# Kernel tuning notes

Measured on AMD Instinct MI355X. Metric: run time of the kernel, lower is better.

## Reference

```python
import jax, jax.numpy as jnp
import numpy as np

B, L, F = 512, 30, 64
N_LEADERS, MAX_LAG = 500, 10
H, TOP_K = 64, 5
SCALE = float(H) ** 0.5


def setup_inputs() -> dict:
    key = jax.random.key(0)
    ks = jax.random.split(key, 16)
    s = 0.05
    return {
        "target_seq": jax.random.normal(ks[0], (B, L, F), jnp.float32),
        "leader_raw_features": jax.random.normal(ks[1], (B, N_LEADERS, MAX_LAG, F), jnp.float32),
        # LSTM params (torch gate order i,f,g,o)
        "W_ih": jax.random.normal(ks[2], (4 * H, F), jnp.float32) * s,
        "W_hh": jax.random.normal(ks[3], (4 * H, H), jnp.float32) * s,
        "b_ih": jax.random.normal(ks[4], (4 * H,), jnp.float32) * s,
        "b_hh": jax.random.normal(ks[5], (4 * H,), jnp.float32) * s,
        # attention projections (bias-free)
        "W_Q": jax.random.normal(ks[6], (H, H), jnp.float32) * s,
        "W_K": jax.random.normal(ks[7], (H, F), jnp.float32) * s,
        # predictor MLP: F->H, H->H//2, H//2->1
        "Wp1": jax.random.normal(ks[8], (H, F), jnp.float32) * s,
        "bp1": jax.random.normal(ks[9], (H,), jnp.float32) * s,
        "Wp2": jax.random.normal(ks[10], (H // 2, H), jnp.float32) * s,
        "bp2": jax.random.normal(ks[11], (H // 2,), jnp.float32) * s,
        "Wp3": jax.random.normal(ks[12], (1, H // 2), jnp.float32) * s,
        "bp3": jax.random.normal(ks[13], (1,), jnp.float32) * s,
    }


def _lstm_last_hidden(x, W_ih, W_hh, b_ih, b_hh):
    # x: [B, L, F] -> last hidden state [B, H]
    b = x.shape[0]
    h0 = jnp.zeros((b, W_hh.shape[1]), x.dtype)

    def step(carry, xt):
        h, c = carry
        gates = xt @ W_ih.T + h @ W_hh.T + b_ih + b_hh  # [B, 4H]
        i, f, g, o = jnp.split(gates, 4, axis=-1)
        i = jax.nn.sigmoid(i)
        f = jax.nn.sigmoid(f)
        g = jnp.tanh(g)
        o = jax.nn.sigmoid(o)
        c = f * c + i * g
        h = o * jnp.tanh(c)
        return (h, c), None

    (h_last, _), _ = jax.lax.scan(step, (h0, h0), jnp.swapaxes(x, 0, 1))
    return h_last


def reference(target_seq, leader_raw_features, W_ih, W_hh, b_ih, b_hh,
              W_Q, W_K, Wp1, bp1, Wp2, bp2, Wp3, bp3):
    b = target_seq.shape[0]
    n_leaders, max_lag, feat = leader_raw_features.shape[1:]

    h_last = _lstm_last_hidden(target_seq, W_ih, W_hh, b_ih, b_hh)  # [B,H]
    query = h_last @ W_Q.T  # [B,H]

    # attn[b,n,l] = sum_h query[b,h] * (W_K @ raw[b,n,l])_h, fused to avoid
    # materializing the [B,N,LAG,H] key tensor.
    attn = jnp.einsum('bnlf,hf,bh->bnl', leader_raw_features, W_K, query) / SCALE

    flat_attn = attn.reshape(b, n_leaders * max_lag)
    k = min(TOP_K, flat_attn.shape[1])
    top_values, top_idx = jax.lax.top_k(flat_attn, k)  # [B,k]
    leader_idx = top_idx // max_lag
    lag_idx = top_idx % max_lag
    top_k_indices = jnp.stack([leader_idx, lag_idx], axis=-1)  # [B,k,2]
    top_k_scores = jax.nn.softmax(top_values, axis=-1)  # [B,k]

    raw_flat = leader_raw_features.reshape(b, n_leaders * max_lag, feat)
    selected = jnp.take_along_axis(raw_flat, top_idx[:, :, None], axis=1)  # [B,k,F]
    weighted = jnp.einsum('bkf,bk->bf', selected, top_k_scores)  # [B,F]

    # predictor MLP (dropout is identity in eval)
    h1 = jax.nn.relu(weighted @ Wp1.T + bp1)
    h2 = jax.nn.relu(h1 @ Wp2.T + bp2)
    pred = h2 @ Wp3.T + bp3  # [B,1]
    return pred, top_k_indices, top_k_scores, attn
```

## Files before the change

kernel.cpp:

```cpp
#include <hip/hip_runtime.h>
#include <math.h>

#define B_SZ   512
#define L_SEQ  30
#define F_DIM  64
#define N_LEAD 500
#define MAXLAG 10
#define H_DIM  64
#define NROWS  5000
#define TOPK   5

#define OFF_IDX   512
#define OFF_SCORE 5632
#define OFF_ATTN  8192

typedef float v4f __attribute__((ext_vector_type(4)));

__device__ __forceinline__ float fast_sigmoid(float x) {
    return 1.f / (1.f + __expf(-x));
}
__device__ __forceinline__ float fast_tanh(float x) {
    float ax = fabsf(x);
    float t  = __expf(-2.f * ax);
    float r  = (1.f - t) / (1.f + t);
    return copysignf(r, x);
}

__device__ __forceinline__ float dot16(const float4* __restrict__ w,
                                       const float4* __restrict__ v) {
    float a0 = 0.f, a1 = 0.f, a2 = 0.f, a3 = 0.f;
#pragma unroll
    for (int k = 0; k < 16; k += 4) {
        a0 += w[k+0].x*v[k+0].x + w[k+0].y*v[k+0].y + w[k+0].z*v[k+0].z + w[k+0].w*v[k+0].w;
        a1 += w[k+1].x*v[k+1].x + w[k+1].y*v[k+1].y + w[k+1].z*v[k+1].z + w[k+1].w*v[k+1].w;
        a2 += w[k+2].x*v[k+2].x + w[k+2].y*v[k+2].y + w[k+2].z*v[k+2].z + w[k+2].w*v[k+2].w;
        a3 += w[k+3].x*v[k+3].x + w[k+3].y*v[k+3].y + w[k+3].z*v[k+3].z + w[k+3].w*v[k+3].w;
    }
    return (a0 + a1) + (a2 + a3);
}

__global__ __launch_bounds__(256) void lstm_kq_kernel(
    const float* __restrict__ x,
    const float* __restrict__ W_ih,
    const float* __restrict__ W_hh,
    const float* __restrict__ b_ih,
    const float* __restrict__ b_hh,
    const float* __restrict__ W_Q,
    const float* __restrict__ W_K,
    float* __restrict__ kq)
{
    __shared__ __align__(16) float xs[L_SEQ * F_DIM];
    __shared__ __align__(16) float hs[H_DIM];
    __shared__ __align__(16) float gates[256];

    const int b = blockIdx.x;
    const int t = threadIdx.x;

    for (int i = t; i < L_SEQ * F_DIM; i += 256)
        xs[i] = x[b * L_SEQ * F_DIM + i];
    if (t < H_DIM) hs[t] = 0.f;

    float4 wih[16], whh[16];
    const float4* wihp = (const float4*)(W_ih + t * 64);
    const float4* whhp = (const float4*)(W_hh + t * 64);
#pragma unroll
    for (int k = 0; k < 16; ++k) { wih[k] = wihp[k]; whh[k] = whhp[k]; }
    const float bsum = b_ih[t] + b_hh[t];

    float c = 0.f;
    __syncthreads();

    float gx = bsum + dot16(wih, (const float4*)xs);

    for (int step = 0; step < L_SEQ; ++step) {
        float g = gx + dot16(whh, (const float4*)hs);
        gates[t] = g;
        __syncthreads();
        if (t < H_DIM) {
            float ig = fast_sigmoid(gates[t]);
            float fg = fast_sigmoid(gates[t + 64]);
            float gg = fast_tanh(gates[t + 128]);
            float og = fast_sigmoid(gates[t + 192]);
            c = fg * c + ig * gg;
            hs[t] = og * fast_tanh(c);
        }
        if (step + 1 < L_SEQ)
            gx = bsum + dot16(wih, (const float4*)(xs + (step + 1) * F_DIM));
        __syncthreads();
    }

    if (t < H_DIM)
        gates[t] = dot16((const float4*)(W_Q + t * 64), (const float4*)hs);
    __syncthreads();
    if (t < F_DIM) {
        float a0 = 0.f, a1 = 0.f;
        for (int h = 0; h < H_DIM; h += 2) {
            a0 += gates[h]     * W_K[h * F_DIM + t];
            a1 += gates[h + 1] * W_K[(h + 1) * F_DIM + t];
        }
        kq[b * F_DIM + t] = a0 + a1;
    }
}

#define CHUNKS 10
#define ROWS_PER_BLK 500
__global__ __launch_bounds__(256) void attn_kernel(
    const float* __restrict__ raw,
    const float* __restrict__ kq,
    float* __restrict__ attn)
{
    const int b     = blockIdx.x / CHUNKS;
    const int chunk = blockIdx.x % CHUNKS;
    const int sub   = threadIdx.x & 15;
    const int rg    = threadIdx.x >> 4;

    const float4 kqv = ((const float4*)(kq + b * 64))[sub];
    const int base   = chunk * ROWS_PER_BLK;
    const size_t rowb = (size_t)b * NROWS;

    for (int it = 0; it < 8; ++it) {
#pragma unroll
        for (int j = 0; j < 4; ++j) {
            int row = base + it * 64 + j * 16 + rg;
            if (row < base + ROWS_PER_BLK) {
                const v4f* pp = (const v4f*)(raw + ((rowb + row) << 6)) + sub;
                v4f v = __builtin_nontemporal_load(pp);
                float s = v.x * kqv.x + v.y * kqv.y + v.z * kqv.z + v.w * kqv.w;
                s += __shfl_xor(s, 8);
                s += __shfl_xor(s, 4);
                s += __shfl_xor(s, 2);
                s += __shfl_xor(s, 1);
                if (sub == 0) attn[rowb + row] = s * 0.125f;
            }
        }
    }
}

__global__ __launch_bounds__(256) void topk_mlp_kernel(
    const float* __restrict__ attn,
    const float* __restrict__ raw,
    const float* __restrict__ Wp1, const float* __restrict__ bp1,
    const float* __restrict__ Wp2, const float* __restrict__ bp2,
    const float* __restrict__ Wp3, const float* __restrict__ bp3,
    float* __restrict__ out)
{
    __shared__ __align__(16) float av[NROWS];
    __shared__ float redv[4];
    __shared__ int   redi[4];
    __shared__ float topv[TOPK];
    __shared__ int   topi[TOPK];
    __shared__ float sc[TOPK];
    __shared__ __align__(16) float wsum[64];
    __shared__ __align__(16) float h1[64];
    __shared__ float h2[32];

    const int b = blockIdx.x, t = threadIdx.x;

    const float4* ain = (const float4*)(attn + (size_t)b * NROWS);
    float4* av4 = (float4*)av;
    for (int i = t; i < NROWS / 4; i += 256) av4[i] = ain[i];
    __syncthreads();

    for (int pp = 0; pp < TOPK; ++pp) {
        float bv = -INFINITY; int bi = 0x7fffffff;
        for (int i = t; i < NROWS; i += 256) {
            float v = av[i];
            if (v > bv || (v == bv && i < bi)) { bv = v; bi = i; }
        }
#pragma unroll
        for (int m = 32; m >= 1; m >>= 1) {
            float ov = __shfl_xor(bv, m);
            int   oi = __shfl_xor(bi, m);
            if (ov > bv || (ov == bv && oi < bi)) { bv = ov; bi = oi; }
        }
        if ((t & 63) == 0) { redv[t >> 6] = bv; redi[t >> 6] = bi; }
        __syncthreads();
        if (t == 0) {
            for (int w = 1; w < 4; ++w)
                if (redv[w] > bv || (redv[w] == bv && redi[w] < bi)) { bv = redv[w]; bi = redi[w]; }
            topv[pp] = bv; topi[pp] = bi;
            av[bi] = -INFINITY;
        }
        __syncthreads();
    }

    if (t == 0) {
        float mx = topv[0];
        float e[TOPK], s = 0.f;
#pragma unroll
        for (int k = 0; k < TOPK; ++k) { e[k] = __expf(topv[k] - mx); s += e[k]; }
        float inv = 1.f / s;
#pragma unroll
        for (int k = 0; k < TOPK; ++k) {
            sc[k] = e[k] * inv;
            out[OFF_IDX + b * 10 + 2 * k]     = (float)(topi[k] / MAXLAG);
            out[OFF_IDX + b * 10 + 2 * k + 1] = (float)(topi[k] % MAXLAG);
            out[OFF_SCORE + b * TOPK + k]     = sc[k];
        }
    }
    __syncthreads();

    if (t < 64) {
        float acc = 0.f;
#pragma unroll
        for (int k = 0; k < TOPK; ++k)
            acc += sc[k] * raw[((size_t)b * NROWS + topi[k]) * 64 + t];
        wsum[t] = acc;
    }
    __syncthreads();
    if (t < 64) {
        float a = bp1[t];
        const float4* w = (const float4*)(Wp1 + t * 64);
        const float4* v = (const float4*)wsum;
#pragma unroll
        for (int k = 0; k < 16; ++k)
            a += w[k].x*v[k].x + w[k].y*v[k].y + w[k].z*v[k].z + w[k].w*v[k].w;
        h1[t] = fmaxf(a, 0.f);
    }
    __syncthreads();
    if (t < 32) {
        float a = bp2[t];
        const float4* w = (const float4*)(Wp2 + t * 64);
        const float4* v = (const float4*)h1;
#pragma unroll
        for (int k = 0; k < 16; ++k)
            a += w[k].x*v[k].x + w[k].y*v[k].y + w[k].z*v[k].z + w[k].w*v[k].w;
        h2[t] = fmaxf(a, 0.f);
    }
    __syncthreads();
    if (t == 0) {
        float a = bp3[0];
#pragma unroll
        for (int f = 0; f < 32; ++f) a += Wp3[f] * h2[f];
        out[b] = a;
    }
}

extern "C" void kernel_launch(void* const* d_in, const int* in_sizes, int n_in,
                              void* d_out, int out_size, void* d_ws, size_t ws_size,
                              hipStream_t stream) {
    const float* target = (const float*)d_in[0];
    const float* raw    = (const float*)d_in[1];
    const float* W_ih   = (const float*)d_in[2];
    const float* W_hh   = (const float*)d_in[3];
    const float* b_ih   = (const float*)d_in[4];
    const float* b_hh   = (const float*)d_in[5];
    const float* W_Q    = (const float*)d_in[6];
    const float* W_K    = (const float*)d_in[7];
    const float* Wp1    = (const float*)d_in[8];
    const float* bp1    = (const float*)d_in[9];
    const float* Wp2    = (const float*)d_in[10];
    const float* bp2    = (const float*)d_in[11];
    const float* Wp3    = (const float*)d_in[12];
    const float* bp3    = (const float*)d_in[13];

    float* out      = (float*)d_out;
    float* kq       = (float*)d_ws;
    float* attn_out = out + OFF_ATTN;

    hipLaunchKernelGGL(lstm_kq_kernel, dim3(B_SZ), dim3(256), 0, stream,
                       target, W_ih, W_hh, b_ih, b_hh, W_Q, W_K, kq);
    hipLaunchKernelGGL(attn_kernel, dim3(B_SZ * CHUNKS), dim3(256), 0, stream,
                       raw, kq, attn_out);
    hipLaunchKernelGGL(topk_mlp_kernel, dim3(B_SZ), dim3(256), 0, stream,
                       attn_out, raw, Wp1, bp1, Wp2, bp2, Wp3, bp3, out);
}
```

Baseline: 188.8 us.

## Fuse per-chunk top-k into attention kernel and merge partial candidates

The attention kernel now keeps each 500-row chunk's scores in shared memory and computes a local top-5 per block, writing candidates to workspace. The final kernel merges 50 candidates per batch with wavefront shuffles instead of re-reading 5000 attention scores and scanning them serially five times. Loads are also issued eight at a time before reducing, to keep more memory requests in flight. The cost is extra shared memory and barriers in the bandwidth-bound attention kernel.

New measurement: 193.2 us. 2.3% more time.

```diff
diff --git a/kernel.cpp b/kernel.cpp
--- a/kernel.cpp
+++ b/kernel.cpp
@@ -9,10 +9,15 @@
 #define H_DIM  64
 #define NROWS  5000
 #define TOPK   5
+#define CHUNKS 10
+#define RPB    500
 
 #define OFF_IDX   512
 #define OFF_SCORE 5632
 #define OFF_ATTN  8192
+
+#define WS_PVAL 32768
+#define WS_PIDX 58368
 
 typedef float v4f __attribute__((ext_vector_type(4)));
 
@@ -41,12 +46,9 @@
 
 __global__ __launch_bounds__(256) void lstm_kq_kernel(
     const float* __restrict__ x,
-    const float* __restrict__ W_ih,
-    const float* __restrict__ W_hh,
-    const float* __restrict__ b_ih,
-    const float* __restrict__ b_hh,
-    const float* __restrict__ W_Q,
-    const float* __restrict__ W_K,
+    const float* __restrict__ W_ih, const float* __restrict__ W_hh,
+    const float* __restrict__ b_ih, const float* __restrict__ b_hh,
+    const float* __restrict__ W_Q,  const float* __restrict__ W_K,
     float* __restrict__ kq)
 {
     __shared__ __align__(16) float xs[L_SEQ * F_DIM];
@@ -102,51 +104,100 @@
     }
 }
 
-#define CHUNKS 10
-#define ROWS_PER_BLK 500
-__global__ __launch_bounds__(256) void attn_kernel(
+__global__ __launch_bounds__(256) void attn_stream_topk_kernel(
     const float* __restrict__ raw,
     const float* __restrict__ kq,
-    float* __restrict__ attn)
+    float* __restrict__ attn,
+    float* __restrict__ pval,
+    int*   __restrict__ pidx)
 {
+    __shared__ __align__(16) float av[512];
+    __shared__ float redv[4];
+    __shared__ int   redi[4];
+
     const int b     = blockIdx.x / CHUNKS;
     const int chunk = blockIdx.x % CHUNKS;
-    const int sub   = threadIdx.x & 15;
-    const int rg    = threadIdx.x >> 4;
+    const int t     = threadIdx.x;
+    const int sub   = t & 15;
+    const int rg    = t >> 4;
 
     const float4 kqv = ((const float4*)(kq + b * 64))[sub];
-    const int base   = chunk * ROWS_PER_BLK;
-    const size_t rowb = (size_t)b * NROWS;
-
-    for (int it = 0; it < 8; ++it) {
-#pragma unroll
-        for (int j = 0; j < 4; ++j) {
-            int row = base + it * 64 + j * 16 + rg;
-            if (row < base + ROWS_PER_BLK) {
-                const v4f* pp = (const v4f*)(raw + ((rowb + row) << 6)) + sub;
-                v4f v = __builtin_nontemporal_load(pp);
-                float s = v.x * kqv.x + v.y * kqv.y + v.z * kqv.z + v.w * kqv.w;
-                s += __shfl_xor(s, 8);
-                s += __shfl_xor(s, 4);
-                s += __shfl_xor(s, 2);
-                s += __shfl_xor(s, 1);
-                if (sub == 0) attn[rowb + row] = s * 0.125f;
-            }
-        }
-    }
-}
-
-__global__ __launch_bounds__(256) void topk_mlp_kernel(
-    const float* __restrict__ attn,
+    const int base = chunk * RPB;
+    const float* rawb  = raw  + (size_t)b * NROWS * 64;
+    float*       attng = attn + (size_t)b * NROWS + base;
+
+    if (t < 12) av[500 + t] = -INFINITY;
+
+#define ISSUE(vk, off) v4f vk = __builtin_nontemporal_load( \
+        (const v4f*)(rawb + (size_t)(base + (off) + rg) * 64) + sub);
+#define REDUCE(vk, off) { \
+    float s = vk.x*kqv.x + vk.y*kqv.y + vk.z*kqv.z + vk.w*kqv.w; \
+    s += __shfl_xor(s, 8); s += __shfl_xor(s, 4); \
+    s += __shfl_xor(s, 2); s += __shfl_xor(s, 1); \
+    if (sub == 0) { float sv = s * 0.125f; int lr = (off) + rg; \
+        av[lr] = sv; __builtin_nontemporal_store(sv, attng + lr); } }
+
+#pragma unroll 1
+    for (int p = 0; p < 384; p += 128) {
+        ISSUE(v0, p +  0) ISSUE(v1, p + 16) ISSUE(v2, p + 32) ISSUE(v3, p + 48)
+        ISSUE(v4, p + 64) ISSUE(v5, p + 80) ISSUE(v6, p + 96) ISSUE(v7, p +112)
+        REDUCE(v0, p +  0) REDUCE(v1, p + 16) REDUCE(v2, p + 32) REDUCE(v3, p + 48)
+        REDUCE(v4, p + 64) REDUCE(v5, p + 80) REDUCE(v6, p + 96) REDUCE(v7, p +112)
+    }
+    {
+        ISSUE(v0, 384) ISSUE(v1, 400) ISSUE(v2, 416) ISSUE(v3, 432)
+        REDUCE(v0, 384) REDUCE(v1, 400) REDUCE(v2, 416) REDUCE(v3, 432)
+    }
+    {
+        ISSUE(v0, 448) ISSUE(v1, 464) ISSUE(v2, 480)
+        int lr = 496 + rg;
+        int safe = lr < RPB ? lr : RPB - 1;
+        v4f v3 = __builtin_nontemporal_load(
+            (const v4f*)(rawb + (size_t)(base + safe) * 64) + sub);
+        REDUCE(v0, 448) REDUCE(v1, 464) REDUCE(v2, 480)
+        float s = v3.x*kqv.x + v3.y*kqv.y + v3.z*kqv.z + v3.w*kqv.w;
+        s += __shfl_xor(s, 8); s += __shfl_xor(s, 4);
+        s += __shfl_xor(s, 2); s += __shfl_xor(s, 1);
+        if (sub == 0 && lr < RPB) { float sv = s * 0.125f;
+            av[lr] = sv; __builtin_nontemporal_store(sv, attng + lr); }
+    }
+#undef ISSUE
+#undef REDUCE
+    __syncthreads();
+
+    float* pv = pval + (size_t)blockIdx.x * TOPK;
+    int*   pi = pidx + (size_t)blockIdx.x * TOPK;
+    for (int p = 0; p < TOPK; ++p) {
+        float v0 = av[t], v1 = av[t + 256];
+        float bv; int bi;
+        if (v1 > v0) { bv = v1; bi = t + 256; } else { bv = v0; bi = t; }
+#pragma unroll
+        for (int m = 32; m >= 1; m >>= 1) {
+            float ov = __shfl_xor(bv, m);
+            int   oi = __shfl_xor(bi, m);
+            if (ov > bv || (ov == bv && oi < bi)) { bv = ov; bi = oi; }
+        }
+        if ((t & 63) == 0) { redv[t >> 6] = bv; redi[t >> 6] = bi; }
+        __syncthreads();
+        if (t == 0) {
+            for (int w = 1; w < 4; ++w)
+                if (redv[w] > bv || (redv[w] == bv && redi[w] < bi)) { bv = redv[w]; bi = redi[w]; }
+            pv[p] = bv; pi[p] = base + bi;
+            av[bi] = -INFINITY;
+        }
+        __syncthreads();
+    }
+}
+
+__global__ __launch_bounds__(256) void merge_mlp_kernel(
+    const float* __restrict__ pval,
+    const int*   __restrict__ pidx,
     const float* __restrict__ raw,
     const float* __restrict__ Wp1, const float* __restrict__ bp1,
     const float* __restrict__ Wp2, const float* __restrict__ bp2,
     const float* __restrict__ Wp3, const float* __restrict__ bp3,
     float* __restrict__ out)
 {
-    __shared__ __align__(16) float av[NROWS];
-    __shared__ float redv[4];
-    __shared__ int   redi[4];
     __shared__ float topv[TOPK];
     __shared__ int   topi[TOPK];
     __shared__ float sc[TOPK];
@@ -156,33 +207,24 @@
 
     const int b = blockIdx.x, t = threadIdx.x;
 
-    const float4* ain = (const float4*)(attn + (size_t)b * NROWS);
-    float4* av4 = (float4*)av;
-    for (int i = t; i < NROWS / 4; i += 256) av4[i] = ain[i];
-    __syncthreads();
-
-    for (int pp = 0; pp < TOPK; ++pp) {
-        float bv = -INFINITY; int bi = 0x7fffffff;
-        for (int i = t; i < NROWS; i += 256) {
-            float v = av[i];
-            if (v > bv || (v == bv && i < bi)) { bv = v; bi = i; }
-        }
-#pragma unroll
-        for (int m = 32; m >= 1; m >>= 1) {
-            float ov = __shfl_xor(bv, m);
-            int   oi = __shfl_xor(bi, m);
-            if (ov > bv || (ov == bv && oi < bi)) { bv = ov; bi = oi; }
-        }
-        if ((t & 63) == 0) { redv[t >> 6] = bv; redi[t >> 6] = bi; }
-        __syncthreads();
-        if (t == 0) {
-            for (int w = 1; w < 4; ++w)
-                if (redv[w] > bv || (redv[w] == bv && redi[w] < bi)) { bv = redv[w]; bi = redi[w]; }
-            topv[pp] = bv; topi[pp] = bi;
-            av[bi] = -INFINITY;
-        }
-        __syncthreads();
-    }
+    if (t < 64) {
+        float v  = -INFINITY;
+        int   idx = 0x7fffffff;
+        if (t < CHUNKS * TOPK) { v = pval[b * 50 + t]; idx = pidx[b * 50 + t]; }
+#pragma unroll
+        for (int p = 0; p < TOPK; ++p) {
+            float bv = v; int bi = idx;
+#pragma unroll
+            for (int m = 32; m >= 1; m >>= 1) {
+                float ov = __shfl_xor(bv, m);
+                int   oi = __shfl_xor(bi, m);
+                if (ov > bv || (ov == bv && oi < bi)) { bv = ov; bi = oi; }
+            }
+            if (t == 0) { topv[p] = bv; topi[p] = bi; }
+            if (idx == bi) v = -INFINITY;
+        }
+    }
+    __syncthreads();
 
     if (t == 0) {
         float mx = topv[0];
@@ -200,11 +242,12 @@
     }
     __syncthreads();
 
+    const float* rawb = raw + (size_t)b * NROWS * 64;
     if (t < 64) {
         float acc = 0.f;
 #pragma unroll
         for (int k = 0; k < TOPK; ++k)
-            acc += sc[k] * raw[((size_t)b * NROWS + topi[k]) * 64 + t];
+            acc += sc[k] * rawb[(size_t)topi[k] * 64 + t];
         wsum[t] = acc;
     }
     __syncthreads();
@@ -254,14 +297,17 @@
     const float* Wp3    = (const float*)d_in[12];
     const float* bp3    = (const float*)d_in[13];
 
-    float* out      = (float*)d_out;
-    float* kq       = (float*)d_ws;
+    float* out  = (float*)d_out;
+    float* ws   = (float*)d_ws;
+    float* kq   = ws;
+    float* pval = ws + WS_PVAL;
+    int*   pidx = (int*)(ws + WS_PIDX);
     float* attn_out = out + OFF_ATTN;
 
     hipLaunchKernelGGL(lstm_kq_kernel, dim3(B_SZ), dim3(256), 0, stream,
                        target, W_ih, W_hh, b_ih, b_hh, W_Q, W_K, kq);
-    hipLaunchKernelGGL(attn_kernel, dim3(B_SZ * CHUNKS), dim3(256), 0, stream,
-                       raw, kq, attn_out);
-    hipLaunchKernelGGL(topk_mlp_kernel, dim3(B_SZ), dim3(256), 0, stream,
-                       attn_out, raw, Wp1, bp1, Wp2, bp2, Wp3, bp3, out);
-}
+    hipLaunchKernelGGL(attn_stream_topk_kernel, dim3(B_SZ * CHUNKS), dim3(256), 0, stream,
+                       raw, kq, attn_out, pval, pidx);
+    hipLaunchKernelGGL(merge_mlp_kernel, dim3(B_SZ), dim3(256), 0, stream,
+                       pval, pidx, raw, Wp1, bp1, Wp2, bp2, Wp3, bp3, out);
+}
```
